# Optimization experiments

Measured on AMD Instinct MI355X. Metric: run time of the kernel, lower is better.

The kernel has to match this reference:

```python
import jax, jax.numpy as jnp
import numpy as np

B, S, D, H = 4, 2048, 1024, 16
DK = D // H
NEG = -1.0e9

def setup_inputs() -> dict:
    key = jax.random.key(0)
    ks = jax.random.split(key, 9)
    scale = 1.0 / np.sqrt(D)
    x = jax.random.normal(ks[0], (B, S, D), dtype=jnp.float32)
    # causal mask: positions with mask==0 are filled with -1e9
    mask = jnp.tril(jnp.ones((S, S), dtype=jnp.int32))[None, None]  # [1,1,S,S]
    Wq = jax.random.normal(ks[1], (D, D), dtype=jnp.float32) * scale
    bq = jax.random.normal(ks[2], (D,), dtype=jnp.float32) * 0.01
    Wk = jax.random.normal(ks[3], (D, D), dtype=jnp.float32) * scale
    bk = jax.random.normal(ks[4], (D,), dtype=jnp.float32) * 0.01
    Wv = jax.random.normal(ks[5], (D, D), dtype=jnp.float32) * scale
    bv = jax.random.normal(ks[6], (D,), dtype=jnp.float32) * 0.01
    Wo = jax.random.normal(ks[7], (D, D), dtype=jnp.float32) * scale
    bo = jax.random.normal(ks[8], (D,), dtype=jnp.float32) * 0.01
    return {"x": x, "mask": mask, "Wq": Wq, "bq": bq, "Wk": Wk, "bk": bk,
            "Wv": Wv, "bv": bv, "Wo": Wo, "bo": bo}

def reference(x, mask, Wq, bq, Wk, bk, Wv, bv, Wo, bo):
    Bb, Ss, Dd = x.shape
    q = (x @ Wq.T + bq).reshape(Bb, Ss, H, DK).transpose(0, 2, 1, 3)  # [B,H,S,DK]
    k = (x @ Wk.T + bk).reshape(Bb, Ss, H, DK).transpose(0, 2, 1, 3)
    v = (x @ Wv.T + bv).reshape(Bb, Ss, H, DK).transpose(0, 2, 1, 3)
    scaled = jnp.einsum('bhqd,bhkd->bhqk', q, k) / jnp.sqrt(jnp.float32(DK))
    scaled = jnp.where(mask == 0, jnp.float32(NEG), scaled)
    attn = jax.nn.softmax(scaled, axis=-1)  # dropout prob = 0 -> identity
    vals = jnp.einsum('bhqk,bhkd->bhqd', attn, v)  # [B,H,S,DK]
    vals = vals.transpose(0, 2, 1, 3).reshape(Bb, Ss, H * DK)
    out = vals @ Wo.T + bo
    return out
```

## Files before the change

### kernel.cpp

```cpp
#include <hip/hip_runtime.h>
#include <hip/hip_bf16.h>
#include <cstdint>

#define B_ 4
#define S_ 2048
#define D_ 1024
#define H_ 16
#define DK_ 64

typedef _Float16 h8 __attribute__((ext_vector_type(8)));
typedef _Float16 h4 __attribute__((ext_vector_type(4)));
typedef _Float16 h2 __attribute__((ext_vector_type(2)));
typedef float f32x4 __attribute__((ext_vector_type(4)));
typedef unsigned int u32x4 __attribute__((ext_vector_type(4)));

__device__ __forceinline__ void gload16(const void* src, void* lds) {
  __builtin_amdgcn_global_load_lds((const __attribute__((address_space(1))) void*)src,
                                   (__attribute__((address_space(3))) void*)lds, 16, 0, 0);
}

__global__ __launch_bounds__(256) void conv_f16(const float* __restrict__ src,
                                                _Float16* __restrict__ dst, int n8) {
  int i = blockIdx.x * 256 + threadIdx.x;
  if (i < n8) {
    int base = i * 8;
    h8 o;
#pragma unroll
    for (int j = 0; j < 8; ++j) o[j] = (_Float16)src[base + j];
    *(h8*)(dst + base) = o;
  }
}

__global__ __launch_bounds__(256) void conv_weights(
    const float* __restrict__ Wq, const float* __restrict__ Wk,
    const float* __restrict__ Wv, const float* __restrict__ Wo,
    const float* __restrict__ bq, const float* __restrict__ bk,
    const float* __restrict__ bv,
    _Float16* __restrict__ wqkv, _Float16* __restrict__ wo,
    float* __restrict__ bqkv) {
  int i = blockIdx.x * 256 + threadIdx.x;
  int seg = i >> 17, r = i & 131071;
  const float* src = seg == 0 ? Wq : seg == 1 ? Wk : seg == 2 ? Wv : Wo;
  int base = r * 8;
  h8 o;
#pragma unroll
  for (int j = 0; j < 8; ++j) o[j] = (_Float16)src[base + j];
  if (seg < 3)
    *(h8*)(wqkv + (size_t)seg * 1048576 + base) = o;
  else
    *(h8*)(wo + base) = o;
  if (i < 768) {
    int bsel = i >> 8, k = (i & 255) * 4;
    const float* bs = bsel == 0 ? bq : bsel == 1 ? bk : bv;
    float4 v = *(const float4*)(bs + k);
    *(float4*)(bqkv + bsel * 1024 + k) = v;
  }
}

template <int MODE>
__global__ __launch_bounds__(256) void gemm_nt(const _Float16* __restrict__ A,
                                               const _Float16* __restrict__ Bw,
                                               const float* __restrict__ bias,
                                               void* __restrict__ Cout,
                                               _Float16* __restrict__ Vt) {
  constexpr int K = D_;
  __shared__ unsigned short lds[2 * 128 * 64];
  char* ldsA = (char*)lds;
  char* ldsB = (char*)(lds + 128 * 64);

  const int tid = threadIdx.x;
  const int w = tid >> 6, lane = tid & 63, g = lane >> 4, c = lane & 15;
  const int wr = w >> 1, wc = w & 1;
  const int bn = blockIdx.x;
  const int bm = blockIdx.y;

  f32x4 acc[4][4] = {};

  const int srow = tid >> 3;
  const int scolsw = ((tid & 7) * 16) ^ ((srow & 7) << 4);
  const char* Ab = (const char*)(A + (size_t)bm * 128 * K);
  const char* Bb = (const char*)(Bw + (size_t)bn * 128 * K);
  const char* Asrc[4];
  const char* Bsrc[4];
#pragma unroll
  for (int j = 0; j < 4; ++j) {
    int row = j * 32 + srow;
    Asrc[j] = Ab + (size_t)row * (K * 2) + scolsw;
    Bsrc[j] = Bb + (size_t)row * (K * 2) + scolsw;
  }
  char* dstA = ldsA + w * 1024;
  char* dstB = ldsB + w * 1024;

  for (int k0 = 0; k0 < K; k0 += 64) {
    __syncthreads();
#pragma unroll
    for (int j = 0; j < 4; ++j) {
      gload16(Asrc[j] + k0 * 2, dstA + j * 4096);
      gload16(Bsrc[j] + k0 * 2, dstB + j * 4096);
    }
    __syncthreads();
#pragma unroll
    for (int kk = 0; kk < 2; ++kk) {
      h8 a[4], b[4];
#pragma unroll
      for (int mi = 0; mi < 4; ++mi) {
        int row = wr * 64 + mi * 16 + c;
        int off = row * 128 + kk * 64 + g * 16;
        a[mi] = *(const h8*)(ldsA + (off ^ ((row & 7) << 4)));
      }
#pragma unroll
      for (int ni = 0; ni < 4; ++ni) {
        int row = wc * 64 + ni * 16 + c;
        int off = row * 128 + kk * 64 + g * 16;
        b[ni] = *(const h8*)(ldsB + (off ^ ((row & 7) << 4)));
      }
      __builtin_amdgcn_s_setprio(1);
#pragma unroll
      for (int mi = 0; mi < 4; ++mi)
#pragma unroll
        for (int ni = 0; ni < 4; ++ni)
          acc[mi][ni] = __builtin_amdgcn_mfma_f32_16x16x32_f16(a[mi], b[ni], acc[mi][ni], 0, 0, 0);
      __builtin_amdgcn_s_setprio(0);
    }
  }

  if (MODE == 0 && bn >= 16) {
#pragma unroll
    for (int mi = 0; mi < 4; ++mi)
#pragma unroll
      for (int ni = 0; ni < 4; ++ni) {
        int m0 = bm * 128 + wr * 64 + mi * 16 + g * 4;
        int n = bn * 128 + wc * 64 + ni * 16 + c;
        float bb = bias[n];
        h4 v4;
#pragma unroll
        for (int r = 0; r < 4; ++r) v4[r] = (_Float16)(acc[mi][ni][r] + bb);
        int bI = m0 >> 11, sI = m0 & 2047;
        int dk = n & 63, hh = (n >> 6) & 15;
        *(h4*)(Vt + (((size_t)(bI * 16 + hh) * 64 + dk) * 2048 + sI)) = v4;
      }
  } else {
#pragma unroll
    for (int mi = 0; mi < 4; ++mi)
#pragma unroll
      for (int ni = 0; ni < 4; ++ni)
#pragma unroll
        for (int r = 0; r < 4; ++r) {
          int m = bm * 128 + wr * 64 + mi * 16 + g * 4 + r;
          int n = bn * 128 + wc * 64 + ni * 16 + c;
          float v = acc[mi][ni][r] + bias[n];
          if (MODE == 0) {
            int which = n >> 10, nn = n & 1023;
            int bI = m >> 11, sI = m & 2047, hI = nn >> 6, dkI = nn & 63;
            ((_Float16*)Cout)[(size_t)which * 8388608 +
                              (((size_t)bI * H_ + hI) * S_ + sI) * DK_ + dkI] = (_Float16)v;
          } else {
            ((float*)Cout)[(size_t)m * D_ + n] = v;
          }
        }
  }
}

__global__ __launch_bounds__(256, 4) void attn_fwd(const _Float16* __restrict__ Q,
                                                   const _Float16* __restrict__ K,
                                                   const _Float16* __restrict__ Vt,
                                                   _Float16* __restrict__ vals) {
  __shared__ unsigned short ldsK[2 * 64 * 64];
  __shared__ unsigned short ldsV[2 * 64 * 64];
  __shared__ unsigned short ldsP[4 * 16 * 64];
  char* pK = (char*)ldsK;
  char* pV = (char*)ldsV;
  char* pP = (char*)ldsP;

  const int tid = threadIdx.x;
  const int w = tid >> 6, lane = tid & 63, g = lane >> 4, c = lane & 15;
  const int bid = blockIdx.x;
  const int pi = bid >> 6;
  const int bh = bid & 63;
  const int bI = bh >> 4, hI = bh & 15;
  const int q0 = pi, q1 = 31 - pi;

  const char* Qb = (const char*)(Q + (size_t)bh * S_ * DK_);
  const char* Kb = (const char*)(K + (size_t)bh * S_ * DK_);
  const char* Vtb = (const char*)(Vt + (size_t)bh * DK_ * S_);

  const int srow = tid >> 3;
  const int scol = (tid & 7) * 16;
  int offK[2], offV[2];
#pragma unroll
  for (int j = 0; j < 2; ++j) {
    int row = j * 32 + srow;
    int colsw = scol ^ ((row & 7) << 4);
    offK[j] = row * 128 + colsw;
    offV[j] = row * 4096 + colsw;
  }
  char* dstK = pK + w * 1024;
  char* dstV = pV + w * 1024;

  auto stage = [&](int buf, int kv0) {
#pragma unroll
    for (int j = 0; j < 2; ++j) {
      gload16(Kb + (size_t)kv0 * 128 + offK[j], dstK + buf * 8192 + j * 4096);
      gload16(Vtb + (size_t)kv0 * 2 + offV[j], dstV + buf * 8192 + j * 4096);
    }
  };

  const _Float16 qsc = (_Float16)(0.125f * 1.44269504f);
  h8 qf[2][2];
#pragma unroll
  for (int gi = 0; gi < 2; ++gi) {
    int qsub = gi ? q1 : q0;
    int qr = qsub * 64 + w * 16 + c;
#pragma unroll
    for (int kk = 0; kk < 2; ++kk) {
      h8 v = *(const h8*)(Qb + (size_t)qr * 128 + kk * 64 + g * 16);
#pragma unroll
      for (int j = 0; j < 8; ++j) v[j] *= qsc;
      qf[gi][kk] = v;
    }
  }

  f32x4 o0[4] = {}, o1[4] = {};
  float m0v = -1e30f, l0v = 0.f, m1v = -1e30f, l1v = 0.f;

  const int nt = q1 + 1;
  stage(0, 0);
  __syncthreads();

  const int sw = (c & 7) << 4;

  for (int t = 0; t < nt; ++t) {
    const int cur = t & 1;
    if (t + 1 < nt) stage(cur ^ 1, (t + 1) * 64);
    const char* bK = pK + cur * 8192;
    const char* bV = pV + cur * 8192;
    const bool g0on = (t <= q0);

    f32x4 s0[4] = {}, s1[4] = {};
#pragma unroll
    for (int kk = 0; kk < 2; ++kk) {
      h8 kfx[4];
#pragma unroll
      for (int ni = 0; ni < 4; ++ni) {
        int row = ni * 16 + c;
        kfx[ni] = *(const h8*)(bK + ((row * 128 + kk * 64 + g * 16) ^ sw));
      }
      __builtin_amdgcn_s_setprio(1);
#pragma unroll
      for (int ni = 0; ni < 4; ++ni)
        s1[ni] = __builtin_amdgcn_mfma_f32_16x16x32_f16(kfx[ni], qf[1][kk], s1[ni], 0, 0, 0);
      if (g0on)
#pragma unroll
        for (int ni = 0; ni < 4; ++ni)
          s0[ni] = __builtin_amdgcn_mfma_f32_16x16x32_f16(kfx[ni], qf[0][kk], s0[ni], 0, 0, 0);
      __builtin_amdgcn_s_setprio(0);
    }

    auto dogroup = [&](f32x4(&s)[4], f32x4(&og)[4], float& mm, float& ll, bool diag) {
      if (diag) {
#pragma unroll
        for (int ni = 0; ni < 4; ++ni)
#pragma unroll
          for (int r = 0; r < 4; ++r) {
            int kv = ni * 16 + g * 4 + r;
            if (kv > w * 16 + c) s[ni][r] = -1e30f;
          }
      }
      float m4[4];
#pragma unroll
      for (int ni = 0; ni < 4; ++ni)
        m4[ni] = fmaxf(fmaxf(s[ni][0], s[ni][1]), fmaxf(s[ni][2], s[ni][3]));
      float pmax = fmaxf(fmaxf(m4[0], m4[1]), fmaxf(m4[2], m4[3]));
      if (!__all(pmax <= mm + 8.f)) {
        float rm = fmaxf(pmax, __shfl_xor(pmax, 16));
        rm = fmaxf(rm, __shfl_xor(rm, 32));
        float mn = fmaxf(mm, rm);
        float al = __builtin_amdgcn_exp2f(mm - mn);
        mm = mn;
        ll *= al;
#pragma unroll
        for (int r = 0; r < 4; ++r) {
          float alr = __shfl(al, g * 4 + r);
#pragma unroll
          for (int nd = 0; nd < 4; ++nd) og[nd][r] *= alr;
        }
      }
      const float mn = mm;
      float rs = 0.f;
#pragma unroll
      for (int ni = 0; ni < 4; ++ni) {
        float e0 = __builtin_amdgcn_exp2f(s[ni][0] - mn);
        float e1 = __builtin_amdgcn_exp2f(s[ni][1] - mn);
        float e2 = __builtin_amdgcn_exp2f(s[ni][2] - mn);
        float e3 = __builtin_amdgcn_exp2f(s[ni][3] - mn);
        rs += (e0 + e1) + (e2 + e3);
        h2 lo = __builtin_bit_cast(h2, __builtin_amdgcn_cvt_pkrtz(e0, e1));
        h2 hi = __builtin_bit_cast(h2, __builtin_amdgcn_cvt_pkrtz(e2, e3));
        h4 pk4 = {lo[0], lo[1], hi[0], hi[1]};
        int off = w * 2048 + c * 128 + ni * 32 + g * 8;
        *(h4*)(pP + (off ^ sw)) = pk4;
      }
      ll += rs;

#pragma unroll
      for (int kk = 0; kk < 2; ++kk) {
        h8 pf = *(const h8*)(pP + ((w * 2048 + c * 128 + kk * 64 + g * 16) ^ sw));
        h8 vf[4];
#pragma unroll
        for (int nd = 0; nd < 4; ++nd) {
          int row = nd * 16 + c;
          vf[nd] = *(const h8*)(bV + ((row * 128 + kk * 64 + g * 16) ^ sw));
        }
        __builtin_amdgcn_s_setprio(1);
#pragma unroll
        for (int nd = 0; nd < 4; ++nd)
          og[nd] = __builtin_amdgcn_mfma_f32_16x16x32_f16(pf, vf[nd], og[nd], 0, 0, 0);
        __builtin_amdgcn_s_setprio(0);
      }
    };

    if (g0on) dogroup(s0, o0, m0v, l0v, t == q0);
    dogroup(s1, o1, m1v, l1v, t == q1);

    __syncthreads();
  }

  auto epi = [&](f32x4(&og)[4], float ll, int qsub) {
    float lt = ll + __shfl_xor(ll, 16);
    lt += __shfl_xor(lt, 32);
    float linv = 1.0f / lt;
#pragma unroll
    for (int r = 0; r < 4; ++r) {
      float inv = __shfl(linv, g * 4 + r);
      int qrow = qsub * 64 + w * 16 + g * 4 + r;
#pragma unroll
      for (int nd = 0; nd < 4; ++nd) {
        int col = hI * 64 + nd * 16 + c;
        vals[((size_t)bI * S_ + qrow) * D_ + col] = (_Float16)(og[nd][r] * inv);
      }
    }
  };
  epi(o0, l0v, q0);
  epi(o1, l1v, q1);
}

extern "C" void kernel_launch(void* const* d_in, const int* in_sizes, int n_in,
                              void* d_out, int out_size, void* d_ws, size_t ws_size,
                              hipStream_t stream) {
  const float* x  = (const float*)d_in[0];
  const float* Wq = (const float*)d_in[2];
  const float* bq = (const float*)d_in[3];
  const float* Wk = (const float*)d_in[4];
  const float* bk = (const float*)d_in[5];
  const float* Wv = (const float*)d_in[6];
  const float* bv = (const float*)d_in[7];
  const float* Wo = (const float*)d_in[8];
  const float* bo = (const float*)d_in[9];
  float* out = (float*)d_out;

  char* ws = (char*)d_ws;
  size_t off = 0;
  auto alloc = [&](size_t bytes) {
    char* p = ws + off;
    off += (bytes + 255) & ~(size_t)255;
    return p;
  };
  _Float16* xb   = (_Float16*)alloc((size_t)B_ * S_ * D_ * 2);
  _Float16* wqkv = (_Float16*)alloc((size_t)3 * D_ * D_ * 2);
  _Float16* wob  = (_Float16*)alloc((size_t)D_ * D_ * 2);
  float*    bqkv = (float*)alloc((size_t)3 * D_ * 4);
  _Float16* qkvw = (_Float16*)alloc((size_t)2 * B_ * H_ * S_ * DK_ * 2);
  _Float16* Vtw  = (_Float16*)alloc((size_t)B_ * H_ * S_ * DK_ * 2);
  _Float16* valw = (_Float16*)alloc((size_t)B_ * S_ * D_ * 2);

  const int nx8 = B_ * S_ * D_ / 8;
  conv_f16<<<(nx8 + 255) / 256, 256, 0, stream>>>(x, xb, nx8);
  conv_weights<<<2048, 256, 0, stream>>>(Wq, Wk, Wv, Wo, bq, bk, bv, wqkv, wob, bqkv);

  gemm_nt<0><<<dim3(24, 64), 256, 0, stream>>>(xb, wqkv, bqkv, qkvw, Vtw);

  attn_fwd<<<1024, 256, 0, stream>>>(qkvw, qkvw + (size_t)8388608, Vtw, valw);

  gemm_nt<1><<<dim3(8, 64), 256, 0, stream>>>(valw, wob, bo, out, nullptr);
}
```

Measured before the change: 194.7 us.

## Merge conversion kernels and serialize attention query tiles into two phases

Fuses the x and weight fp16 conversion kernels into one launch to save a kernel launch. In attention, the two query tiles per block are now processed one after the other, each with its own KV loop, instead of sharing one loop over K/V tiles. This lowers register pressure (the launch-bounds occupancy hint is dropped). The PV product is split into two halves interleaved with the exp computation. The cost is that K/V tiles for the shorter tile are loaded twice rather than shared.

```diff
diff --git a/kernel.cpp b/kernel.cpp
--- a/kernel.cpp
+++ b/kernel.cpp
@@ -19,41 +19,39 @@
                                    (__attribute__((address_space(3))) void*)lds, 16, 0, 0);
 }
 
-__global__ __launch_bounds__(256) void conv_f16(const float* __restrict__ src,
-                                                _Float16* __restrict__ dst, int n8) {
-  int i = blockIdx.x * 256 + threadIdx.x;
-  if (i < n8) {
-    int base = i * 8;
-    h8 o;
-#pragma unroll
-    for (int j = 0; j < 8; ++j) o[j] = (_Float16)src[base + j];
-    *(h8*)(dst + base) = o;
-  }
-}
-
-__global__ __launch_bounds__(256) void conv_weights(
+__global__ __launch_bounds__(256) void conv_all(
+    const float* __restrict__ x,
     const float* __restrict__ Wq, const float* __restrict__ Wk,
     const float* __restrict__ Wv, const float* __restrict__ Wo,
     const float* __restrict__ bq, const float* __restrict__ bk,
     const float* __restrict__ bv,
-    _Float16* __restrict__ wqkv, _Float16* __restrict__ wo,
-    float* __restrict__ bqkv) {
-  int i = blockIdx.x * 256 + threadIdx.x;
-  int seg = i >> 17, r = i & 131071;
-  const float* src = seg == 0 ? Wq : seg == 1 ? Wk : seg == 2 ? Wv : Wo;
-  int base = r * 8;
-  h8 o;
-#pragma unroll
-  for (int j = 0; j < 8; ++j) o[j] = (_Float16)src[base + j];
-  if (seg < 3)
-    *(h8*)(wqkv + (size_t)seg * 1048576 + base) = o;
-  else
-    *(h8*)(wo + base) = o;
-  if (i < 768) {
-    int bsel = i >> 8, k = (i & 255) * 4;
-    const float* bs = bsel == 0 ? bq : bsel == 1 ? bk : bv;
-    float4 v = *(const float4*)(bs + k);
-    *(float4*)(bqkv + bsel * 1024 + k) = v;
+    _Float16* __restrict__ xb, _Float16* __restrict__ wqkv,
+    _Float16* __restrict__ wo, float* __restrict__ bqkv) {
+  const int bid = blockIdx.x, tid = threadIdx.x;
+  if (bid < 4096) {
+    int base = (bid * 256 + tid) * 8;
+    h8 o;
+#pragma unroll
+    for (int j = 0; j < 8; ++j) o[j] = (_Float16)x[base + j];
+    *(h8*)(xb + base) = o;
+  } else {
+    int i = (bid - 4096) * 256 + tid;
+    int seg = i >> 17, r = i & 131071;
+    const float* src = seg == 0 ? Wq : seg == 1 ? Wk : seg == 2 ? Wv : Wo;
+    int base = r * 8;
+    h8 o;
+#pragma unroll
+    for (int j = 0; j < 8; ++j) o[j] = (_Float16)src[base + j];
+    if (seg < 3)
+      *(h8*)(wqkv + (size_t)seg * 1048576 + base) = o;
+    else
+      *(h8*)(wo + base) = o;
+    if (i < 768) {
+      int bsel = i >> 8, k = (i & 255) * 4;
+      const float* bs = bsel == 0 ? bq : bsel == 1 ? bk : bv;
+      float4 v = *(const float4*)(bs + k);
+      *(float4*)(bqkv + bsel * 1024 + k) = v;
+    }
   }
 }
 
@@ -161,10 +159,10 @@
   }
 }
 
-__global__ __launch_bounds__(256, 4) void attn_fwd(const _Float16* __restrict__ Q,
-                                                   const _Float16* __restrict__ K,
-                                                   const _Float16* __restrict__ Vt,
-                                                   _Float16* __restrict__ vals) {
+__global__ __launch_bounds__(256) void attn_fwd(const _Float16* __restrict__ Q,
+                                                const _Float16* __restrict__ K,
+                                                const _Float16* __restrict__ Vt,
+                                                _Float16* __restrict__ vals) {
   __shared__ unsigned short ldsK[2 * 64 * 64];
   __shared__ unsigned short ldsV[2 * 64 * 64];
   __shared__ unsigned short ldsP[4 * 16 * 64];
@@ -206,58 +204,51 @@
   };
 
   const _Float16 qsc = (_Float16)(0.125f * 1.44269504f);
-  h8 qf[2][2];
-#pragma unroll
-  for (int gi = 0; gi < 2; ++gi) {
-    int qsub = gi ? q1 : q0;
-    int qr = qsub * 64 + w * 16 + c;
+  const int sw = (c & 7) << 4;
+
+  for (int phase = 0; phase < 2; ++phase) {
+    const int qsub = (phase == 0) ? q0 : q1;
+    const int qw0 = qsub * 64 + w * 16;
+
+    h8 qf[2];
 #pragma unroll
     for (int kk = 0; kk < 2; ++kk) {
-      h8 v = *(const h8*)(Qb + (size_t)qr * 128 + kk * 64 + g * 16);
+      h8 v = *(const h8*)(Qb + (size_t)(qw0 + c) * 128 + kk * 64 + g * 16);
 #pragma unroll
       for (int j = 0; j < 8; ++j) v[j] *= qsc;
-      qf[gi][kk] = v;
-    }
-  }
-
-  f32x4 o0[4] = {}, o1[4] = {};
-  float m0v = -1e30f, l0v = 0.f, m1v = -1e30f, l1v = 0.f;
-
-  const int nt = q1 + 1;
-  stage(0, 0);
-  __syncthreads();
-
-  const int sw = (c & 7) << 4;
-
-  for (int t = 0; t < nt; ++t) {
-    const int cur = t & 1;
-    if (t + 1 < nt) stage(cur ^ 1, (t + 1) * 64);
-    const char* bK = pK + cur * 8192;
-    const char* bV = pV + cur * 8192;
-    const bool g0on = (t <= q0);
-
-    f32x4 s0[4] = {}, s1[4] = {};
-#pragma unroll
-    for (int kk = 0; kk < 2; ++kk) {
-      h8 kfx[4];
-#pragma unroll
-      for (int ni = 0; ni < 4; ++ni) {
-        int row = ni * 16 + c;
-        kfx[ni] = *(const h8*)(bK + ((row * 128 + kk * 64 + g * 16) ^ sw));
-      }
-      __builtin_amdgcn_s_setprio(1);
-#pragma unroll
-      for (int ni = 0; ni < 4; ++ni)
-        s1[ni] = __builtin_amdgcn_mfma_f32_16x16x32_f16(kfx[ni], qf[1][kk], s1[ni], 0, 0, 0);
-      if (g0on)
+      qf[kk] = v;
+    }
+
+    f32x4 o[4] = {};
+    float m_ = -1e30f, l_ = 0.f;
+
+    const int nt = qsub + 1;
+    stage(0, 0);
+    __syncthreads();
+
+    for (int t = 0; t < nt; ++t) {
+      const int cur = t & 1;
+      if (t + 1 < nt) stage(cur ^ 1, (t + 1) * 64);
+      const char* bK = pK + cur * 8192;
+      const char* bV = pV + cur * 8192;
+
+      f32x4 s[4] = {};
+#pragma unroll
+      for (int kk = 0; kk < 2; ++kk) {
+        h8 kfx[4];
+#pragma unroll
+        for (int ni = 0; ni < 4; ++ni) {
+          int row = ni * 16 + c;
+          kfx[ni] = *(const h8*)(bK + ((row * 128 + kk * 64 + g * 16) ^ sw));
+        }
+        __builtin_amdgcn_s_setprio(1);
 #pragma unroll
         for (int ni = 0; ni < 4; ++ni)
-          s0[ni] = __builtin_amdgcn_mfma_f32_16x16x32_f16(kfx[ni], qf[0][kk], s0[ni], 0, 0, 0);
-      __builtin_amdgcn_s_setprio(0);
-    }
-
-    auto dogroup = [&](f32x4(&s)[4], f32x4(&og)[4], float& mm, float& ll, bool diag) {
-      if (diag) {
+          s[ni] = __builtin_amdgcn_mfma_f32_16x16x32_f16(kfx[ni], qf[kk], s[ni], 0, 0, 0);
+        __builtin_amdgcn_s_setprio(0);
+      }
+
+      if (t == nt - 1) {
 #pragma unroll
         for (int ni = 0; ni < 4; ++ni)
 #pragma unroll
@@ -266,29 +257,31 @@
             if (kv > w * 16 + c) s[ni][r] = -1e30f;
           }
       }
+
       float m4[4];
 #pragma unroll
       for (int ni = 0; ni < 4; ++ni)
         m4[ni] = fmaxf(fmaxf(s[ni][0], s[ni][1]), fmaxf(s[ni][2], s[ni][3]));
       float pmax = fmaxf(fmaxf(m4[0], m4[1]), fmaxf(m4[2], m4[3]));
-      if (!__all(pmax <= mm + 8.f)) {
+      if (!__all(pmax <= m_ + 8.f)) {
         float rm = fmaxf(pmax, __shfl_xor(pmax, 16));
         rm = fmaxf(rm, __shfl_xor(rm, 32));
-        float mn = fmaxf(mm, rm);
-        float al = __builtin_amdgcn_exp2f(mm - mn);
-        mm = mn;
-        ll *= al;
+        float mn = fmaxf(m_, rm);
+        float al = __builtin_amdgcn_exp2f(m_ - mn);
+        m_ = mn;
+        l_ *= al;
 #pragma unroll
         for (int r = 0; r < 4; ++r) {
           float alr = __shfl(al, g * 4 + r);
 #pragma unroll
-          for (int nd = 0; nd < 4; ++nd) og[nd][r] *= alr;
-        }
-      }
-      const float mn = mm;
+          for (int nd = 0; nd < 4; ++nd) o[nd][r] *= alr;
+        }
+      }
+      const float mn = m_;
       float rs = 0.f;
-#pragma unroll
-      for (int ni = 0; ni < 4; ++ni) {
+
+#pragma unroll
+      for (int ni = 0; ni < 2; ++ni) {
         float e0 = __builtin_amdgcn_exp2f(s[ni][0] - mn);
         float e1 = __builtin_amdgcn_exp2f(s[ni][1] - mn);
         float e2 = __builtin_amdgcn_exp2f(s[ni][2] - mn);
@@ -300,33 +293,53 @@
         int off = w * 2048 + c * 128 + ni * 32 + g * 8;
         *(h4*)(pP + (off ^ sw)) = pk4;
       }
-      ll += rs;
-
-#pragma unroll
-      for (int kk = 0; kk < 2; ++kk) {
-        h8 pf = *(const h8*)(pP + ((w * 2048 + c * 128 + kk * 64 + g * 16) ^ sw));
+      {
+        h8 pf = *(const h8*)(pP + ((w * 2048 + c * 128 + g * 16) ^ sw));
         h8 vf[4];
 #pragma unroll
         for (int nd = 0; nd < 4; ++nd) {
           int row = nd * 16 + c;
-          vf[nd] = *(const h8*)(bV + ((row * 128 + kk * 64 + g * 16) ^ sw));
+          vf[nd] = *(const h8*)(bV + ((row * 128 + g * 16) ^ sw));
         }
         __builtin_amdgcn_s_setprio(1);
 #pragma unroll
         for (int nd = 0; nd < 4; ++nd)
-          og[nd] = __builtin_amdgcn_mfma_f32_16x16x32_f16(pf, vf[nd], og[nd], 0, 0, 0);
+          o[nd] = __builtin_amdgcn_mfma_f32_16x16x32_f16(pf, vf[nd], o[nd], 0, 0, 0);
         __builtin_amdgcn_s_setprio(0);
       }
-    };
-
-    if (g0on) dogroup(s0, o0, m0v, l0v, t == q0);
-    dogroup(s1, o1, m1v, l1v, t == q1);
-
-    __syncthreads();
-  }
-
-  auto epi = [&](f32x4(&og)[4], float ll, int qsub) {
-    float lt = ll + __shfl_xor(ll, 16);
+#pragma unroll
+      for (int ni = 2; ni < 4; ++ni) {
+        float e0 = __builtin_amdgcn_exp2f(s[ni][0] - mn);
+        float e1 = __builtin_amdgcn_exp2f(s[ni][1] - mn);
+        float e2 = __builtin_amdgcn_exp2f(s[ni][2] - mn);
+        float e3 = __builtin_amdgcn_exp2f(s[ni][3] - mn);
+        rs += (e0 + e1) + (e2 + e3);
+        h2 lo = __builtin_bit_cast(h2, __builtin_amdgcn_cvt_pkrtz(e0, e1));
+        h2 hi = __builtin_bit_cast(h2, __builtin_amdgcn_cvt_pkrtz(e2, e3));
+        h4 pk4 = {lo[0], lo[1], hi[0], hi[1]};
+        int off = w * 2048 + c * 128 + ni * 32 + g * 8;
+        *(h4*)(pP + (off ^ sw)) = pk4;
+      }
+      {
+        h8 pf = *(const h8*)(pP + ((w * 2048 + c * 128 + 64 + g * 16) ^ sw));
+        h8 vf[4];
+#pragma unroll
+        for (int nd = 0; nd < 4; ++nd) {
+          int row = nd * 16 + c;
+          vf[nd] = *(const h8*)(bV + ((row * 128 + 64 + g * 16) ^ sw));
+        }
+        __builtin_amdgcn_s_setprio(1);
+#pragma unroll
+        for (int nd = 0; nd < 4; ++nd)
+          o[nd] = __builtin_amdgcn_mfma_f32_16x16x32_f16(pf, vf[nd], o[nd], 0, 0, 0);
+        __builtin_amdgcn_s_setprio(0);
+      }
+      l_ += rs;
+
+      __syncthreads();
+    }
+
+    float lt = l_ + __shfl_xor(l_, 16);
     lt += __shfl_xor(lt, 32);
     float linv = 1.0f / lt;
 #pragma unroll
@@ -336,12 +349,10 @@
 #pragma unroll
       for (int nd = 0; nd < 4; ++nd) {
         int col = hI * 64 + nd * 16 + c;
-        vals[((size_t)bI * S_ + qrow) * D_ + col] = (_Float16)(og[nd][r] * inv);
-      }
-    }
-  };
-  epi(o0, l0v, q0);
-  epi(o1, l1v, q1);
+        vals[((size_t)bI * S_ + qrow) * D_ + col] = (_Float16)(o[nd][r] * inv);
+      }
+    }
+  }
 }
 
 extern "C" void kernel_launch(void* const* d_in, const int* in_sizes, int n_in,
@@ -373,9 +384,7 @@
   _Float16* Vtw  = (_Float16*)alloc((size_t)B_ * H_ * S_ * DK_ * 2);
   _Float16* valw = (_Float16*)alloc((size_t)B_ * S_ * D_ * 2);
 
-  const int nx8 = B_ * S_ * D_ / 8;
-  conv_f16<<<(nx8 + 255) / 256, 256, 0, stream>>>(x, xb, nx8);
-  conv_weights<<<2048, 256, 0, stream>>>(Wq, Wk, Wv, Wo, bq, bk, bv, wqkv, wob, bqkv);
+  conv_all<<<6144, 256, 0, stream>>>(x, Wq, Wk, Wv, Wo, bq, bk, bv, xb, wqkv, wob, bqkv);
 
   gemm_nt<0><<<dim3(24, 64), 256, 0, stream>>>(xb, wqkv, bqkv, qkvw, Vtw);
 
```

Measured after the change: 191.9 us. Within noise of the previous version (-1.4%).
